# Performance work log

Measured on AMD Instinct MI355X. Metric: run time of the kernel, lower is better.

Reference implementation:

```python
import jax, jax.numpy as jnp
import numpy as np

NH, NL, NP, GA = 8, 4, 4, 8  # num_heads, num_levels, num_points, grid_align_num
SHAPES = np.array([[128, 128], [64, 64], [32, 32], [16, 16]], dtype=np.int64)  # (W, H) per level


def _grid_sample(img, grid):
    """F.grid_sample bilinear, padding_mode='zeros', align_corners=False.
    img: [N,C,H,W], grid: [N,Hg,Wg,2] in [-1,1] (x,y). Returns [N,C,Hg,Wg]."""
    N, C, H, W = img.shape
    x = (grid[..., 0] + 1.0) * (W * 0.5) - 0.5
    y = (grid[..., 1] + 1.0) * (H * 0.5) - 0.5
    x0 = jnp.floor(x)
    y0 = jnp.floor(y)
    wx = (x - x0)[:, None]  # [N,1,Hg,Wg]
    wy = (y - y0)[:, None]
    x0i = x0.astype(jnp.int32)
    y0i = y0.astype(jnp.int32)
    img_flat = img.reshape(N, C, H * W)
    Hg, Wg = grid.shape[1], grid.shape[2]

    def tap(ix, iy):
        valid = (ix >= 0) & (ix < W) & (iy >= 0) & (iy < H)
        lin = jnp.clip(iy, 0, H - 1) * W + jnp.clip(ix, 0, W - 1)
        v = jnp.take_along_axis(img_flat, lin.reshape(N, 1, Hg * Wg), axis=2)
        return v.reshape(N, C, Hg, Wg) * valid[:, None].astype(img.dtype)

    v00 = tap(x0i, y0i)
    v01 = tap(x0i + 1, y0i)
    v10 = tap(x0i, y0i + 1)
    v11 = tap(x0i + 1, y0i + 1)
    return (v00 * (1 - wx) * (1 - wy) + v01 * wx * (1 - wy)
            + v10 * (1 - wx) * wy + v11 * wx * wy)


def setup_inputs() -> dict:
    key = jax.random.key(0)
    ks = jax.random.split(key, 6)
    bs, nq, E = 2, 16384, 256
    total = int((SHAPES[:, 0] * SHAPES[:, 1]).sum())  # 21760
    query = jax.random.normal(ks[0], (bs, nq, E), jnp.float32)
    value = jax.random.normal(ks[1], (bs, total, NH, E // NH), jnp.float32)
    reference_points = jax.random.uniform(ks[2], (bs, nq, 1, NL * 2), jnp.float32)
    W_off = jax.random.normal(ks[3], (NH * NL * NP * 2, E), jnp.float32) * 0.01
    # structured offset bias per init_weights (directional rays, radius ~ point index)
    thetas = jnp.arange(NH, dtype=jnp.float32) * (2.0 * np.pi / NH)
    gi = jnp.stack([jnp.cos(thetas), jnp.sin(thetas)], -1)  # [NH,2]
    gi = gi / jnp.max(jnp.abs(gi), axis=-1, keepdims=True)
    gi = jnp.tile(gi[:, None, None, :], (1, NL, NP, 1))
    gi = gi * jnp.arange(1, NP + 1, dtype=jnp.float32)[None, None, :, None]
    b_off = gi.reshape(-1)
    W_attn = jax.random.normal(ks[4], (NH * NL * NP, E), jnp.float32) * 0.01
    b_attn = jax.random.normal(ks[5], (NH * NL * NP,), jnp.float32) * 0.01
    return {"query": query, "value": value, "reference_points": reference_points,
            "W_off": W_off, "b_off": b_off, "W_attn": W_attn, "b_attn": b_attn,
            "spatial_shapes": np.asarray(SHAPES)}


def reference(query, value, reference_points, W_off, b_off, W_attn, b_attn, spatial_shapes):
    bs, nq, E = query.shape
    d = E // NH
    shapes = np.asarray(spatial_shapes)  # static [L,2] (W,H)

    # sampling offsets and locations (non-deploy path)
    off = (query @ W_off.T + b_off).reshape(bs, nq, NH, NL * NP * 2)
    ref = jnp.tile(reference_points, (1, 1, NH, NP)).reshape(bs, nq, NH, NL * NP * 2)
    # offset_normalizer: (1/spatial_shapes).repeat(1, NP).flatten() -> layout (l, p, xy)
    norm = jnp.asarray(np.tile(1.0 / shapes.astype(np.float32), (1, NP)).reshape(-1))
    loc = (ref + off * norm) * 2.0 - 1.0  # [bs, nq, NH, NL*NP*2]

    # attention weights: softmax over levels*points, regrouped to (L, G, P) layout
    attn = jax.nn.softmax((query @ W_attn.T + b_attn).reshape(bs, nq, NH, NL * NP), axis=-1)
    attn = (attn.reshape(bs, nq // GA, GA, NH, NL, NP)
            .transpose(0, 3, 1, 4, 2, 5)
            .reshape(bs * NH, 1, nq // GA, NL * GA * NP))

    grids = loc.reshape(bs, nq, NH, NL, NP, 2)
    outs = []
    start = 0
    for lvl in range(NL):
        W_, H_ = int(shapes[lvl, 0]), int(shapes[lvl, 1])
        n = H_ * W_
        v = value[:, start:start + n].transpose(0, 2, 3, 1).reshape(bs * NH, d, H_, W_)
        start += n
        g = grids[:, :, :, lvl].transpose(0, 2, 1, 3, 4).reshape(bs * NH, nq // GA, GA * NP, 2)
        outs.append(_grid_sample(v, g))  # [bs*NH, d, nq//GA, GA*NP]
    samp = jnp.concatenate(outs, axis=-1) * attn  # [bs*NH, d, nq//GA, NL*GA*NP]
    # reduce_sum linear with fixed 0/1 weight == sum over levels and points per group slot
    out = samp.reshape(bs * NH, d, nq // GA, NL, GA, NP).sum(axis=(3, 5))
    return out.reshape(bs, NH * d, nq)
```

## Files before the change

kernel.cpp:

```cpp
#include <hip/hip_runtime.h>
#include <hip/hip_bf16.h>


typedef __attribute__((ext_vector_type(4))) float    float4v;
typedef __attribute__((ext_vector_type(8))) _Float16 half8;
typedef __attribute__((ext_vector_type(4))) _Float16 half4;
typedef __attribute__((ext_vector_type(2))) _Float16 half2v;

#define NQ    16384
#define NTOK  21760
#define LREC  48

#define GEMM_BLOCKS 768
#define CONV_BLOCKS 10880

union H8 { half8 v; half2v p[4]; };

#define LDSTR 88
__global__ __launch_bounds__(256) void fused_kernel(
    const float* __restrict__ qf,
    const float* __restrict__ Woff, const float* __restrict__ Wattn,
    const float* __restrict__ boff, const float* __restrict__ battn,
    const float* __restrict__ val,
    _Float16* __restrict__ lh, _Float16* __restrict__ vh) {
  const int tid = threadIdx.x;

  if (blockIdx.x >= GEMM_BLOCKS) {
    int i = (blockIdx.x - GEMM_BLOCKS) * 256 + tid;
    float4v v = ((const float4v*)val)[i];
    half4 o;
    o[0] = (_Float16)v[0]; o[1] = (_Float16)v[1];
    o[2] = (_Float16)v[2]; o[3] = (_Float16)v[3];
    ((half4*)vh)[i] = o;
    return;
  }

  __shared__ _Float16 As[128 * LDSTR];
  __shared__ _Float16 Bs[128 * LDSTR];

  const int lane = tid & 63;
  const int wv   = tid >> 6;
  const int wm   = wv >> 1, wn = wv & 1;
  const int quad = lane >> 4;
  const int r    = lane & 15;
  const int blockM = (blockIdx.x & 255) * 128;
  const int n0     = (blockIdx.x >> 8) * 128;

  float4v acc[4][4];
#pragma unroll
  for (int i = 0; i < 4; ++i)
#pragma unroll
    for (int j = 0; j < 4; ++j) acc[i][j] = (float4v){0.f, 0.f, 0.f, 0.f};

  for (int kc = 0; kc < 4; ++kc) {
    const int k0 = kc * 64;
    if (kc) __syncthreads();
#pragma unroll
    for (int it = 0; it < 8; ++it) {
      int idx = it * 256 + tid;
      int row = idx >> 4, k4 = idx & 15;
      float4v v = *(const float4v*)(qf + (size_t)(blockM + row) * 256 + k0 + k4 * 4);
      half4 o;
      o[0] = (_Float16)v[0]; o[1] = (_Float16)v[1];
      o[2] = (_Float16)v[2]; o[3] = (_Float16)v[3];
      *(half4*)&As[row * LDSTR + k4 * 4] = o;
    }
#pragma unroll
    for (int it = 0; it < 8; ++it) {
      int idx = it * 256 + tid;
      int row = idx >> 4, k4 = idx & 15;
      int n = n0 + row;
      const float* src = (n < 256) ? (Woff + (size_t)n * 256)
                                   : (Wattn + (size_t)(n - 256) * 256);
      float4v v = *(const float4v*)(src + k0 + k4 * 4);
      half4 o;
      o[0] = (_Float16)v[0]; o[1] = (_Float16)v[1];
      o[2] = (_Float16)v[2]; o[3] = (_Float16)v[3];
      *(half4*)&Bs[row * LDSTR + k4 * 4] = o;
    }
    __syncthreads();

#pragma unroll
    for (int kf = 0; kf < 2; ++kf) {
      const int ko = kf * 32 + quad * 8;
      half8 af[4], bf[4];
#pragma unroll
      for (int mi = 0; mi < 4; ++mi)
        af[mi] = *(const half8*)&As[(wm * 64 + mi * 16 + r) * LDSTR + ko];
#pragma unroll
      for (int ni = 0; ni < 4; ++ni)
        bf[ni] = *(const half8*)&Bs[(wn * 64 + ni * 16 + r) * LDSTR + ko];
#pragma unroll
      for (int mi = 0; mi < 4; ++mi)
#pragma unroll
        for (int ni = 0; ni < 4; ++ni)
          acc[mi][ni] = __builtin_amdgcn_mfma_f32_16x16x32_f16(af[mi], bf[ni], acc[mi][ni], 0, 0, 0);
    }
  }

#pragma unroll
  for (int mi = 0; mi < 4; ++mi) {
    const int mb = blockM + wm * 64 + mi * 16 + quad * 4;
#pragma unroll
    for (int ni = 0; ni < 4; ++ni) {
      const int n = n0 + wn * 64 + ni * 16 + r;
      const float bias = (n < 256) ? boff[n] : battn[n - 256];
      const int h    = (n < 256) ? (n >> 5) : ((n - 256) >> 4);
      const int slot = (n < 256) ? (n & 31) : (32 + ((n - 256) & 15));
#pragma unroll
      for (int reg = 0; reg < 4; ++reg) {
        const int bq = mb + reg;
        const int b = bq >> 14, q = bq & 16383;
        lh[((size_t)(b * 8 + h) * NQ + q) * LREC + slot] =
            (_Float16)(acc[mi][ni][reg] + bias);
      }
    }
  }
}

__global__ __launch_bounds__(256) void sample_kernel(
    const _Float16* __restrict__ vh, const float* __restrict__ refp,
    const _Float16* __restrict__ lh, float* __restrict__ out) {
  const int bid   = blockIdx.x;
  const int xcd   = bid & 7;
  const int local = bid >> 3;
  const int hb    = xcd * 2 + (local >> 10);
  const int qt    = local & 1023;
  const int h     = hb & 7;
  const int b     = hb >> 3;
  const int tid = threadIdx.x;
  const int c4 = tid & 3;
  const int l  = (tid >> 2) & 3;
  const int qi = tid >> 4;
  const int q  = qt * 16 + qi;
  const size_t bq = (size_t)b * NQ + q;
  const _Float16* rec = lh + ((size_t)hb * NQ + q) * LREC;

  const half8 oh = *(const half8*)(rec + l * 8);
  float al[16];
#pragma unroll
  for (int i = 0; i < 2; ++i) {
    half8 ah = *(const half8*)(rec + 32 + i * 8);
#pragma unroll
    for (int j = 0; j < 8; ++j) al[i * 8 + j] = (float)ah[j];
  }
  const half4 ownl = *(const half4*)(rec + 32 + l * 4);

  float mx = -1e30f;
#pragma unroll
  for (int i = 0; i < 16; ++i) mx = fmaxf(mx, al[i]);
  float ssum = 0.f;
#pragma unroll
  for (int i = 0; i < 16; ++i) ssum += __expf(al[i] - mx);
  const float inv = 1.0f / ssum;

  float4v rp0 = *(const float4v*)(refp + bq * 8);
  float4v rp1 = *(const float4v*)(refp + bq * 8 + 4);
  const float rpx[4] = {rp0[0], rp0[2], rp1[0], rp1[2]};
  const float rpy[4] = {rp0[1], rp0[3], rp1[1], rp1[3]};

  const int   W    = 128 >> l;
  const float fW   = (float)W;
  const int   base = (l == 0) ? 0 : (l == 1) ? 16384 : (l == 2) ? 20480 : 21504;
  const _Float16* vlev = vh + (size_t)b * NTOK * 256 + h * 32 + c4 * 8
                            + (size_t)base * 256;

  half2v accl0 = (half2v){(_Float16)0, (_Float16)0};
  half2v accl1 = (half2v){(_Float16)0, (_Float16)0};
  half2v accl2 = (half2v){(_Float16)0, (_Float16)0};
  half2v accl3 = (half2v){(_Float16)0, (_Float16)0};

#pragma unroll
  for (int p = 0; p < 4; ++p) {
    const float a  = __expf((float)ownl[p] - mx) * inv;
    const float ox = (float)oh[p * 2];
    const float oy = (float)oh[p * 2 + 1];
    const float x = rpx[p] * fW + ox - 0.5f;
    const float y = rpy[p] * fW + oy - 0.5f;
    const float xf = floorf(x), yf = floorf(y);
    const float fx = x - xf, fy = y - yf;
    const int ix = (int)xf, iy = (int)yf;
    const int ix0 = min(max(ix, 0), W - 1);
    const int ix1 = min(max(ix + 1, 0), W - 1);
    const int iy0 = min(max(iy, 0), W - 1);
    const int iy1 = min(max(iy + 1, 0), W - 1);
    const float wx0 = ((unsigned)ix       < (unsigned)W) ? 1.f - fx : 0.f;
    const float wx1 = ((unsigned)(ix + 1) < (unsigned)W) ? fx       : 0.f;
    const float wy0 = ((unsigned)iy       < (unsigned)W) ? 1.f - fy : 0.f;
    const float wy1 = ((unsigned)(iy + 1) < (unsigned)W) ? fy       : 0.f;
    const _Float16 w00 = (_Float16)(a * wx0 * wy0);
    const _Float16 w01 = (_Float16)(a * wx1 * wy0);
    const _Float16 w10 = (_Float16)(a * wx0 * wy1);
    const _Float16 w11 = (_Float16)(a * wx1 * wy1);
    const half2v h00 = (half2v){w00, w00};
    const half2v h01 = (half2v){w01, w01};
    const half2v h10 = (half2v){w10, w10};
    const half2v h11 = (half2v){w11, w11};
    const _Float16* r0 = vlev + (size_t)(iy0 * W) * 256;
    const _Float16* r1 = vlev + (size_t)(iy1 * W) * 256;
    H8 t00, t01, t10, t11;
    t00.v = *(const half8*)(r0 + ix0 * 256);
    t01.v = *(const half8*)(r0 + ix1 * 256);
    t10.v = *(const half8*)(r1 + ix0 * 256);
    t11.v = *(const half8*)(r1 + ix1 * 256);
    accl0 += h00 * t00.p[0] + h01 * t01.p[0] + h10 * t10.p[0] + h11 * t11.p[0];
    accl1 += h00 * t00.p[1] + h01 * t01.p[1] + h10 * t10.p[1] + h11 * t11.p[1];
    accl2 += h00 * t00.p[2] + h01 * t01.p[2] + h10 * t10.p[2] + h11 * t11.p[2];
    accl3 += h00 * t00.p[3] + h01 * t01.p[3] + h10 * t10.p[3] + h11 * t11.p[3];
  }

  float acc0[4], acc1[4];
  acc0[0] = (float)accl0[0]; acc0[1] = (float)accl0[1];
  acc0[2] = (float)accl1[0]; acc0[3] = (float)accl1[1];
  acc1[0] = (float)accl2[0]; acc1[1] = (float)accl2[1];
  acc1[2] = (float)accl3[0]; acc1[3] = (float)accl3[1];

  __shared__ float sm[4][16][33];
#pragma unroll
  for (int j = 0; j < 4; ++j) {
    sm[l][qi][c4 * 8 + j]     = acc0[j];
    sm[l][qi][c4 * 8 + 4 + j] = acc1[j];
  }
  __syncthreads();
  const size_t obase = ((size_t)b * 256 + h * 32) * NQ + qt * 16;
#pragma unroll
  for (int i = 0; i < 2; ++i) {
    const int idx = i * 256 + tid;
    const int c  = idx >> 4;
    const int ql = idx & 15;
    const float v = ((sm[0][ql][c] + sm[1][ql][c]) + sm[2][ql][c]) + sm[3][ql][c];
    out[obase + (size_t)c * NQ + ql] = v;
  }
}

extern "C" void kernel_launch(void* const* d_in, const int* in_sizes, int n_in,
                              void* d_out, int out_size, void* d_ws, size_t ws_size,
                              hipStream_t stream) {
  const float* query = (const float*)d_in[0];
  const float* value = (const float*)d_in[1];
  const float* refp  = (const float*)d_in[2];
  const float* Woff  = (const float*)d_in[3];
  const float* boff  = (const float*)d_in[4];
  const float* Wattn = (const float*)d_in[5];
  const float* battn = (const float*)d_in[6];
  float* out = (float*)d_out;

  char* ws = (char*)d_ws;
  _Float16* vh = (_Float16*)ws;
  _Float16* lh = (_Float16*)(ws + 22282240);

  fused_kernel<<<GEMM_BLOCKS + CONV_BLOCKS, 256, 0, stream>>>(
      query, Woff, Wattn, boff, battn, value, lh, vh);
  sample_kernel<<<16384, 256, 0, stream>>>(vh, refp, lh, out);
}
```

Measured before the change: 215.9 us.

## Split value conversion into grid-stride kernel and share softmax via LDS

The fp32-to-fp16 value conversion moves out of the fused GEMM launch into its own grid-stride kernel with fewer blocks. In the sampling kernel, the 16-way softmax per query is now computed once cooperatively: each thread handles one logit, the max and sum are reduced with wave shuffles, and the normalized weights are stored in shared memory. Before, every thread recomputed the full softmax redundantly. The cost is an extra kernel launch, a __syncthreads, and weights rounded to fp16 before use.

```diff
diff --git a/kernel.cpp b/kernel.cpp
--- a/kernel.cpp
+++ b/kernel.cpp
@@ -12,28 +12,18 @@
 #define LREC  48
 
 #define GEMM_BLOCKS 768
-#define CONV_BLOCKS 10880
+#define CONV_GRID   2048
+#define CONV_N4     2785280
 
 union H8 { half8 v; half2v p[4]; };
 
 #define LDSTR 88
-__global__ __launch_bounds__(256) void fused_kernel(
+__global__ __launch_bounds__(256) void gemm_kernel(
     const float* __restrict__ qf,
     const float* __restrict__ Woff, const float* __restrict__ Wattn,
     const float* __restrict__ boff, const float* __restrict__ battn,
-    const float* __restrict__ val,
-    _Float16* __restrict__ lh, _Float16* __restrict__ vh) {
+    _Float16* __restrict__ lh) {
   const int tid = threadIdx.x;
-
-  if (blockIdx.x >= GEMM_BLOCKS) {
-    int i = (blockIdx.x - GEMM_BLOCKS) * 256 + tid;
-    float4v v = ((const float4v*)val)[i];
-    half4 o;
-    o[0] = (_Float16)v[0]; o[1] = (_Float16)v[1];
-    o[2] = (_Float16)v[2]; o[3] = (_Float16)v[3];
-    ((half4*)vh)[i] = o;
-    return;
-  }
 
   __shared__ _Float16 As[128 * LDSTR];
   __shared__ _Float16 Bs[128 * LDSTR];
@@ -118,6 +108,18 @@
   }
 }
 
+__global__ __launch_bounds__(256) void conv_kernel(
+    const float* __restrict__ val, _Float16* __restrict__ vh) {
+  for (int i = blockIdx.x * 256 + threadIdx.x; i < CONV_N4;
+       i += CONV_GRID * 256) {
+    float4v v = ((const float4v*)val)[i];
+    half4 o;
+    o[0] = (_Float16)v[0]; o[1] = (_Float16)v[1];
+    o[2] = (_Float16)v[2]; o[3] = (_Float16)v[3];
+    ((half4*)vh)[i] = o;
+  }
+}
+
 __global__ __launch_bounds__(256) void sample_kernel(
     const _Float16* __restrict__ vh, const float* __restrict__ refp,
     const _Float16* __restrict__ lh, float* __restrict__ out) {
@@ -129,6 +131,27 @@
   const int h     = hb & 7;
   const int b     = hb >> 3;
   const int tid = threadIdx.x;
+
+  __shared__ _Float16 wsm[16][16];
+  {
+    const int q16  = tid >> 4;
+    const int slot = tid & 15;
+    const float lg = (float)lh[((size_t)hb * NQ + qt * 16 + q16) * LREC + 32 + slot];
+    float m = lg;
+    m = fmaxf(m, __shfl_xor(m, 1));
+    m = fmaxf(m, __shfl_xor(m, 2));
+    m = fmaxf(m, __shfl_xor(m, 4));
+    m = fmaxf(m, __shfl_xor(m, 8));
+    const float e = __expf(lg - m);
+    float s = e;
+    s += __shfl_xor(s, 1);
+    s += __shfl_xor(s, 2);
+    s += __shfl_xor(s, 4);
+    s += __shfl_xor(s, 8);
+    wsm[q16][slot] = (_Float16)(e * (1.0f / s));
+  }
+  __syncthreads();
+
   const int c4 = tid & 3;
   const int l  = (tid >> 2) & 3;
   const int qi = tid >> 4;
@@ -137,22 +160,7 @@
   const _Float16* rec = lh + ((size_t)hb * NQ + q) * LREC;
 
   const half8 oh = *(const half8*)(rec + l * 8);
-  float al[16];
-#pragma unroll
-  for (int i = 0; i < 2; ++i) {
-    half8 ah = *(const half8*)(rec + 32 + i * 8);
-#pragma unroll
-    for (int j = 0; j < 8; ++j) al[i * 8 + j] = (float)ah[j];
-  }
-  const half4 ownl = *(const half4*)(rec + 32 + l * 4);
-
-  float mx = -1e30f;
-#pragma unroll
-  for (int i = 0; i < 16; ++i) mx = fmaxf(mx, al[i]);
-  float ssum = 0.f;
-#pragma unroll
-  for (int i = 0; i < 16; ++i) ssum += __expf(al[i] - mx);
-  const float inv = 1.0f / ssum;
+  const half4 ownw = *(const half4*)&wsm[qi][l * 4];
 
   float4v rp0 = *(const float4v*)(refp + bq * 8);
   float4v rp1 = *(const float4v*)(refp + bq * 8 + 4);
@@ -172,7 +180,7 @@
 
 #pragma unroll
   for (int p = 0; p < 4; ++p) {
-    const float a  = __expf((float)ownl[p] - mx) * inv;
+    const float a  = (float)ownw[p];
     const float ox = (float)oh[p * 2];
     const float oy = (float)oh[p * 2 + 1];
     const float x = rpx[p] * fW + ox - 0.5f;
@@ -249,7 +257,8 @@
   _Float16* vh = (_Float16*)ws;
   _Float16* lh = (_Float16*)(ws + 22282240);
 
-  fused_kernel<<<GEMM_BLOCKS + CONV_BLOCKS, 256, 0, stream>>>(
-      query, Woff, Wattn, boff, battn, value, lh, vh);
+  gemm_kernel<<<GEMM_BLOCKS, 256, 0, stream>>>(
+      query, Woff, Wattn, boff, battn, lh);
+  conv_kernel<<<CONV_GRID, 256, 0, stream>>>(value, vh);
   sample_kernel<<<16384, 256, 0, stream>>>(vh, refp, lh, out);
 }
```

Measured after the change: 218.8 us. Within noise of the previous version (+1.3%).
